# Performance work log

Measured on AMD Instinct MI355X. Metric: run time of the kernel, lower is better.

The kernel has to match this reference:

```python
import jax, jax.numpy as jnp
import numpy as np

H = 4    # heads
D = 64   # embed_dim


def setup_inputs() -> dict:
    key = jax.random.key(0)
    ks = jax.random.split(key, 10)
    N, L = 128, 1024
    f = jnp.float32
    return {
        "seq_items": jax.random.normal(ks[0], (N, L, D), f),
        "target_items": jax.random.normal(ks[1], (N, D), f),
        "memory": jax.random.normal(ks[2], (N, D), f),
        # nn.Linear weights stored torch-style [out_features, in_features]
        "Wk": jax.random.normal(ks[3], (H * D, D), f) * 0.1,
        "Wq": jax.random.normal(ks[4], (H * D, D), f) * 0.1,
        "Wv": jax.random.normal(ks[5], (H * D, D), f) * 0.1,
        "Wu": jax.random.normal(ks[6], (D, H * D), f) * 0.1,
        "bu": jnp.zeros((D,), f),
        "W1": jax.random.normal(ks[7], (8, 4 * D), f) * 0.1,
        "b1": jnp.zeros((8,), f),
        "W2": jax.random.normal(ks[8], (1, 8), f) * 0.1,
        "b2": jnp.zeros((1,), f),
    }


def reference(seq_items, target_items, memory, Wk, Wq, Wv, Wu, bu, W1, b1, W2, b2):
    N, L, d = seq_items.shape
    # projections, split into heads: [N, L, H, D]
    e = (seq_items @ Wk.T).reshape(N, L, H, D)
    V = (seq_items @ Wv.T).reshape(N, L, H, D)
    v = (target_items @ Wq.T).reshape(N, 1, H, D)   # broadcast over L
    m = memory.reshape(N, 1, 1, D)                   # broadcast over L and heads
    # np.where(e_, 1, 0): 1 where nonzero
    mask = (e != 0).astype(e.dtype)
    a1 = (v - e) * mask
    a2 = (v * e) * mask
    a3 = (m - e) * mask
    a4 = (m * e) * mask
    alpha = jnp.concatenate([a1, a2, a3, a4], axis=-1)  # [N, L, H, 4D]
    # tiny MLP attention scorer: 4D -> 8 -> 1, sigmoid each
    hmid = jax.nn.sigmoid(alpha @ W1.T + b1)
    att = jax.nn.sigmoid(hmid @ W2.T + b2)              # [N, L, H, 1]
    out = jnp.einsum('nlhq,nlhd->nqhd', att, V).reshape(N, H * D)
    output = out @ Wu.T + bu                            # [N, D]
    return output, att
```

## Files before the change

### kernel.cpp

```cpp
#include <hip/hip_runtime.h>
#include <math.h>

#define NN 128
#define LL 1024
#define HH 4
#define DD 64

typedef __attribute__((ext_vector_type(8))) short short8;
typedef __attribute__((ext_vector_type(4))) float f32x4;

__device__ __forceinline__ float sigm(float x) {
    return __builtin_amdgcn_rcpf(1.f + __expf(-x));
}

__device__ __forceinline__ unsigned short f2bf(float x) {
    union { float f; unsigned u; } v; v.f = x;
    unsigned r = v.u + 0x7FFFu + ((v.u >> 16) & 1u);
    return (unsigned short)(r >> 16);
}

__device__ __forceinline__ short8 pack_bf8(float4 a, float4 b) {
    short8 r;
    r[0] = (short)f2bf(a.x); r[1] = (short)f2bf(a.y);
    r[2] = (short)f2bf(a.z); r[3] = (short)f2bf(a.w);
    r[4] = (short)f2bf(b.x); r[5] = (short)f2bf(b.y);
    r[6] = (short)f2bf(b.z); r[7] = (short)f2bf(b.w);
    return r;
}

__global__ void __launch_bounds__(1024, 4) fused_kernel(
    const float* __restrict__ seq, const float* __restrict__ target,
    const float* __restrict__ memv, const float* __restrict__ Wk,
    const float* __restrict__ Wq, const float* __restrict__ Wv,
    const float* __restrict__ Wu, const float* __restrict__ bu,
    const float* __restrict__ W1, const float* __restrict__ b1,
    const float* __restrict__ W2, const float* __restrict__ b2,
    float* __restrict__ att_out, float* __restrict__ out)
{
    const int n = blockIdx.x;
    const int t = threadIdx.x;
    const int lane = t & 63;
    const int w = t >> 6;

    __shared__ __align__(16) float tl[64];
    __shared__ __align__(16) float ml[64];
    __shared__ float vh[4][64];
    __shared__ float wh[4][512];
    __shared__ float cp[4][64];
    __shared__ float cvl[32];
    __shared__ __align__(16) short wt_lds[32 * 72];
    __shared__ __align__(16) short seq_bf[256 * 72];
    __shared__ __align__(16) float att_l[1024];
    __shared__ __align__(16) float Tp_l[16][256];
    __shared__ float T_l[256];
    __shared__ __align__(16) float U_l[256];
    __shared__ float op[16 * 64];

    const int gg = t >> 8;
    const int tt = t & 255;
    const int h = gg;

    if (t < 64)       tl[t] = target[n * 64 + t];
    else if (t < 128) ml[t - 64] = memv[n * 64 + (t - 64)];
    __syncthreads();

    {
        const int d = tt >> 2, kq = tt & 3;
        const float4* wq4 = reinterpret_cast<const float4*>(Wq + (h * 64 + d) * 64 + kq * 16);
        const float4* tl4 = reinterpret_cast<const float4*>(tl + kq * 16);
        float s = 0.f;
        #pragma unroll
        for (int cc = 0; cc < 4; ++cc) {
            const float4 a = wq4[cc], bb = tl4[cc];
            s = fmaf(a.x, bb.x, s); s = fmaf(a.y, bb.y, s);
            s = fmaf(a.z, bb.z, s); s = fmaf(a.w, bb.w, s);
        }
        s += __shfl_xor(s, 1);
        s += __shfl_xor(s, 2);
        if (kq == 0) vh[h][d] = s;
    }
    __syncthreads();

    {
        const int d = tt & 63, jh = tt >> 6;
        const float vv = vh[h][d], mm = ml[d];
        #pragma unroll
        for (int r = 0; r < 2; ++r) {
            const int j = jh + r * 4;
            float wv = -W1[j * 256 + d] - W1[j * 256 + 128 + d];
            wv = fmaf(W1[j * 256 + 64 + d], vv, wv);
            wv = fmaf(W1[j * 256 + 192 + d], mm, wv);
            wh[h][d * 8 + j] = wv;
        }
    }
    if (tt < 64) {
        const int j = tt >> 3, sl = tt & 7;
        float s = 0.f;
        #pragma unroll
        for (int d8 = 0; d8 < 8; ++d8) {
            const int d = sl * 8 + d8;
            s = fmaf(W1[j * 256 + d], vh[h][d], s);
            s = fmaf(W1[j * 256 + 128 + d], ml[d], s);
        }
        cp[h][tt] = s;
    }
    __syncthreads();
    if (tt < 8) {
        float s = b1[tt];
        #pragma unroll
        for (int sl = 0; sl < 8; ++sl) s += cp[h][tt * 8 + sl];
        cvl[h * 8 + tt] = s;
    }

    {
        const int k = tt & 63, jp = tt >> 6;
        float s0 = 0.f, s1 = 0.f;
        #pragma unroll 8
        for (int d = 0; d < 64; ++d) {
            const float wk = Wk[(h * 64 + d) * 64 + k];
            s0 = fmaf(wk, wh[h][d * 8 + jp], s0);
            s1 = fmaf(wk, wh[h][d * 8 + jp + 4], s1);
        }
        wt_lds[(h * 8 + jp) * 72 + k]     = (short)f2bf(s0);
        wt_lds[(h * 8 + jp + 4) * 72 + k] = (short)f2bf(s1);
    }
    __syncthreads();

    const float* sbase = seq + (size_t)n * LL * 64;

    const int rt = w & 1;
    const int ctA = w >> 1;
    const int g = lane >> 4;
    const int cidx = lane & 15;

    short8 afrag[2];
    #pragma unroll
    for (int ks = 0; ks < 2; ++ks)
        afrag[ks] = *reinterpret_cast<const short8*>(
            wt_lds + (rt * 16 + cidx) * 72 + ks * 32 + g * 8);

    const float4 w2v = *reinterpret_cast<const float4*>(W2 + 4 * (g & 1));
    const float b2v = b2[0];
    const float cv0 = cvl[rt * 16 + g * 4 + 0];
    const float cv1 = cvl[rt * 16 + g * 4 + 1];
    const float cv2 = cvl[rt * 16 + g * 4 + 2];
    const float cv3 = cvl[rt * 16 + g * 4 + 3];

    float th0 = 0.f, th1 = 0.f, th2 = 0.f, th3 = 0.f;

    for (int sc = 0; sc < 4; ++sc) {
        const float* scb = sbase + sc * 256 * 64;

        #pragma unroll
        for (int gsg = 0; gsg < 2; ++gsg) {
            const int p8 = gsg * 1024 + t;
            const int l = p8 >> 3, seg = p8 & 7;
            const float* rp = scb + l * 64 + seg * 8;
            const float4 a = *reinterpret_cast<const float4*>(rp);
            const float4 bb = *reinterpret_cast<const float4*>(rp + 4);
            *reinterpret_cast<short8*>(seq_bf + l * 72 + seg * 8) = pack_bf8(a, bb);
        }
        __syncthreads();

        #pragma unroll
        for (int cc = 0; cc < 2; ++cc) {
            const int ct = ctA + cc * 8;
            const int l = ct * 16 + cidx;
            f32x4 acc;
            acc[0] = cv0; acc[1] = cv1; acc[2] = cv2; acc[3] = cv3;
            const short8 bf0 = *reinterpret_cast<const short8*>(seq_bf + l * 72 + g * 8);
            const short8 bf1 = *reinterpret_cast<const short8*>(seq_bf + l * 72 + 32 + g * 8);
            acc = __builtin_amdgcn_mfma_f32_16x16x32_bf16(afrag[0], bf0, acc, 0, 0, 0);
            acc = __builtin_amdgcn_mfma_f32_16x16x32_bf16(afrag[1], bf1, acc, 0, 0, 0);

            float local = w2v.x * sigm(acc[0]);
            local = fmaf(w2v.y, sigm(acc[1]), local);
            local = fmaf(w2v.z, sigm(acc[2]), local);
            local = fmaf(w2v.w, sigm(acc[3]), local);
            local += __shfl_xor(local, 16);
            const float attv = sigm(b2v + local);
            if ((lane & 16) == 0) {
                const int hh = 2 * rt + (g >> 1);
                att_l[l * 4 + hh] = attv;
            }
        }
        __syncthreads();

        att_out[((size_t)n * LL + sc * 256) * 4 + t] = att_l[t];

        {
            const float* sq = scb + (w * 16) * 64 + lane;
            #pragma unroll 4
            for (int li = 0; li < 16; ++li) {
                const float s = sq[li * 64];
                const float4 a = *reinterpret_cast<const float4*>(att_l + (w * 16 + li) * 4);
                th0 = fmaf(a.x, s, th0); th1 = fmaf(a.y, s, th1);
                th2 = fmaf(a.z, s, th2); th3 = fmaf(a.w, s, th3);
            }
        }
    }

    Tp_l[w][0 * 64 + lane] = th0;
    Tp_l[w][1 * 64 + lane] = th1;
    Tp_l[w][2 * 64 + lane] = th2;
    Tp_l[w][3 * 64 + lane] = th3;
    __syncthreads();

    if (t < 256) {
        float s = 0.f;
        #pragma unroll
        for (int i = 0; i < 16; ++i) s += Tp_l[i][t];
        T_l[t] = s;
    }
    __syncthreads();

    {
        const int hd = t >> 2, kq = t & 3;
        const int hq = hd >> 6;
        const float4* wv4 = reinterpret_cast<const float4*>(Wv + hd * 64 + kq * 16);
        const float4* t4  = reinterpret_cast<const float4*>(T_l + hq * 64 + kq * 16);
        float s = 0.f;
        #pragma unroll
        for (int i = 0; i < 4; ++i) {
            const float4 a = wv4[i], bb = t4[i];
            s = fmaf(a.x, bb.x, s); s = fmaf(a.y, bb.y, s);
            s = fmaf(a.z, bb.z, s); s = fmaf(a.w, bb.w, s);
        }
        s += __shfl_xor(s, 1);
        s += __shfl_xor(s, 2);
        if (kq == 0) U_l[hd] = s;
    }
    __syncthreads();

    {
        const int q = t & 63, qr = t >> 6;
        const float4* wu4 = reinterpret_cast<const float4*>(Wu + q * 256 + qr * 16);
        const float4* u4  = reinterpret_cast<const float4*>(U_l + qr * 16);
        float s = 0.f;
        #pragma unroll
        for (int i = 0; i < 4; ++i) {
            const float4 a = wu4[i], bb = u4[i];
            s = fmaf(a.x, bb.x, s); s = fmaf(a.y, bb.y, s);
            s = fmaf(a.z, bb.z, s); s = fmaf(a.w, bb.w, s);
        }
        op[qr * 64 + q] = s;
    }
    __syncthreads();
    if (t < 64) {
        float s = bu[t];
        #pragma unroll
        for (int qr = 0; qr < 16; ++qr) s += op[qr * 64 + t];
        out[n * 64 + t] = s;
    }
}

extern "C" void kernel_launch(void* const* d_in, const int* in_sizes, int n_in,
                              void* d_out, int out_size, void* d_ws, size_t ws_size,
                              hipStream_t stream) {
    const float* seq    = (const float*)d_in[0];
    const float* target = (const float*)d_in[1];
    const float* memv   = (const float*)d_in[2];
    const float* Wk     = (const float*)d_in[3];
    const float* Wq     = (const float*)d_in[4];
    const float* Wv     = (const float*)d_in[5];
    const float* Wu     = (const float*)d_in[6];
    const float* bu     = (const float*)d_in[7];
    const float* W1     = (const float*)d_in[8];
    const float* b1     = (const float*)d_in[9];
    const float* W2     = (const float*)d_in[10];
    const float* b2     = (const float*)d_in[11];

    float* out = (float*)d_out;
    float* att = out + NN * DD;

    fused_kernel<<<NN, 1024, 0, stream>>>(seq, target, memv, Wk, Wq, Wv, Wu,
                                          bu, W1, b1, W2, b2, att, out);
}
```

Baseline: 25.08 us.

## Split each sequence across four 256-thread blocks with a separate reduction kernel

Each batch row is now split into four blocks of 256 threads, each handling 256 sequence positions, instead of one 1024-thread block per row. The per-head weight preprocessing is recomputed in every block through a serial loop over heads. The second half-chunk of seq is prefetched into registers while the first half is processed. Partial outputs go to workspace and a second small kernel adds them together with the bias. The aim is better CU coverage with 512 smaller blocks, at the cost of redundant preprocessing work, an extra launch and a workspace round trip.

```diff
diff --git a/kernel.cpp b/kernel.cpp
--- a/kernel.cpp
+++ b/kernel.cpp
@@ -1,10 +1,9 @@
 #include <hip/hip_runtime.h>
+#include <hip/hip_bf16.h>
 #include <math.h>
 
 #define NN 128
 #define LL 1024
-#define HH 4
-#define DD 64
 
 typedef __attribute__((ext_vector_type(8))) short short8;
 typedef __attribute__((ext_vector_type(4))) float f32x4;
@@ -13,123 +12,121 @@
     return __builtin_amdgcn_rcpf(1.f + __expf(-x));
 }
 
-__device__ __forceinline__ unsigned short f2bf(float x) {
-    union { float f; unsigned u; } v; v.f = x;
-    unsigned r = v.u + 0x7FFFu + ((v.u >> 16) & 1u);
-    return (unsigned short)(r >> 16);
+__device__ __forceinline__ short bf16s(float x) {
+    __hip_bfloat16 h = __float2bfloat16(x);
+    union { __hip_bfloat16 hh; short s; } u; u.hh = h;
+    return u.s;
 }
 
 __device__ __forceinline__ short8 pack_bf8(float4 a, float4 b) {
     short8 r;
-    r[0] = (short)f2bf(a.x); r[1] = (short)f2bf(a.y);
-    r[2] = (short)f2bf(a.z); r[3] = (short)f2bf(a.w);
-    r[4] = (short)f2bf(b.x); r[5] = (short)f2bf(b.y);
-    r[6] = (short)f2bf(b.z); r[7] = (short)f2bf(b.w);
+    r[0] = bf16s(a.x); r[1] = bf16s(a.y); r[2] = bf16s(a.z); r[3] = bf16s(a.w);
+    r[4] = bf16s(b.x); r[5] = bf16s(b.y); r[6] = bf16s(b.z); r[7] = bf16s(b.w);
     return r;
 }
 
-__global__ void __launch_bounds__(1024, 4) fused_kernel(
+__global__ void __launch_bounds__(256, 2) fused_kernel(
     const float* __restrict__ seq, const float* __restrict__ target,
     const float* __restrict__ memv, const float* __restrict__ Wk,
     const float* __restrict__ Wq, const float* __restrict__ Wv,
-    const float* __restrict__ Wu, const float* __restrict__ bu,
-    const float* __restrict__ W1, const float* __restrict__ b1,
-    const float* __restrict__ W2, const float* __restrict__ b2,
-    float* __restrict__ att_out, float* __restrict__ out)
+    const float* __restrict__ Wu, const float* __restrict__ W1,
+    const float* __restrict__ b1, const float* __restrict__ W2,
+    const float* __restrict__ b2,
+    float* __restrict__ att_out, float* __restrict__ contrib)
 {
-    const int n = blockIdx.x;
+    const int b = blockIdx.x;
+    const int n = b >> 2;
+    const int c = b & 3;
     const int t = threadIdx.x;
     const int lane = t & 63;
     const int w = t >> 6;
 
     __shared__ __align__(16) float tl[64];
     __shared__ __align__(16) float ml[64];
-    __shared__ float vh[4][64];
-    __shared__ float wh[4][512];
-    __shared__ float cp[4][64];
+    __shared__ float vh[64];
+    __shared__ float wh[512];
+    __shared__ float cp[64];
     __shared__ float cvl[32];
     __shared__ __align__(16) short wt_lds[32 * 72];
-    __shared__ __align__(16) short seq_bf[256 * 72];
-    __shared__ __align__(16) float att_l[1024];
-    __shared__ __align__(16) float Tp_l[16][256];
+    __shared__ __align__(16) short seq_bf[128 * 72];
+    __shared__ __align__(16) float att_l[512];
+    __shared__ __align__(16) float Tp_l[4][256];
     __shared__ float T_l[256];
     __shared__ __align__(16) float U_l[256];
-    __shared__ float op[16 * 64];
-
-    const int gg = t >> 8;
-    const int tt = t & 255;
-    const int h = gg;
+    __shared__ float op[256];
 
     if (t < 64)       tl[t] = target[n * 64 + t];
     else if (t < 128) ml[t - 64] = memv[n * 64 + (t - 64)];
     __syncthreads();
 
-    {
-        const int d = tt >> 2, kq = tt & 3;
-        const float4* wq4 = reinterpret_cast<const float4*>(Wq + (h * 64 + d) * 64 + kq * 16);
-        const float4* tl4 = reinterpret_cast<const float4*>(tl + kq * 16);
-        float s = 0.f;
-        #pragma unroll
-        for (int cc = 0; cc < 4; ++cc) {
-            const float4 a = wq4[cc], bb = tl4[cc];
-            s = fmaf(a.x, bb.x, s); s = fmaf(a.y, bb.y, s);
-            s = fmaf(a.z, bb.z, s); s = fmaf(a.w, bb.w, s);
-        }
-        s += __shfl_xor(s, 1);
-        s += __shfl_xor(s, 2);
-        if (kq == 0) vh[h][d] = s;
-    }
-    __syncthreads();
-
-    {
-        const int d = tt & 63, jh = tt >> 6;
-        const float vv = vh[h][d], mm = ml[d];
-        #pragma unroll
-        for (int r = 0; r < 2; ++r) {
-            const int j = jh + r * 4;
-            float wv = -W1[j * 256 + d] - W1[j * 256 + 128 + d];
-            wv = fmaf(W1[j * 256 + 64 + d], vv, wv);
-            wv = fmaf(W1[j * 256 + 192 + d], mm, wv);
-            wh[h][d * 8 + j] = wv;
-        }
-    }
-    if (tt < 64) {
-        const int j = tt >> 3, sl = tt & 7;
-        float s = 0.f;
-        #pragma unroll
-        for (int d8 = 0; d8 < 8; ++d8) {
-            const int d = sl * 8 + d8;
-            s = fmaf(W1[j * 256 + d], vh[h][d], s);
-            s = fmaf(W1[j * 256 + 128 + d], ml[d], s);
-        }
-        cp[h][tt] = s;
-    }
-    __syncthreads();
-    if (tt < 8) {
-        float s = b1[tt];
-        #pragma unroll
-        for (int sl = 0; sl < 8; ++sl) s += cp[h][tt * 8 + sl];
-        cvl[h * 8 + tt] = s;
-    }
-
-    {
-        const int k = tt & 63, jp = tt >> 6;
-        float s0 = 0.f, s1 = 0.f;
-        #pragma unroll 8
-        for (int d = 0; d < 64; ++d) {
-            const float wk = Wk[(h * 64 + d) * 64 + k];
-            s0 = fmaf(wk, wh[h][d * 8 + jp], s0);
-            s1 = fmaf(wk, wh[h][d * 8 + jp + 4], s1);
-        }
-        wt_lds[(h * 8 + jp) * 72 + k]     = (short)f2bf(s0);
-        wt_lds[(h * 8 + jp + 4) * 72 + k] = (short)f2bf(s1);
-    }
-    __syncthreads();
-
-    const float* sbase = seq + (size_t)n * LL * 64;
+    for (int h = 0; h < 4; ++h) {
+        {
+            const int d = t >> 2, kq = t & 3;
+            const float4* wq4 = reinterpret_cast<const float4*>(Wq + (h * 64 + d) * 64 + kq * 16);
+            const float4* tl4 = reinterpret_cast<const float4*>(tl + kq * 16);
+            float s = 0.f;
+            #pragma unroll
+            for (int cc = 0; cc < 4; ++cc) {
+                const float4 a = wq4[cc], bb = tl4[cc];
+                s = fmaf(a.x, bb.x, s); s = fmaf(a.y, bb.y, s);
+                s = fmaf(a.z, bb.z, s); s = fmaf(a.w, bb.w, s);
+            }
+            s += __shfl_xor(s, 1);
+            s += __shfl_xor(s, 2);
+            if (kq == 0) vh[d] = s;
+        }
+        __syncthreads();
+
+        {
+            const int d = t & 63, jh = t >> 6;
+            const float vv = vh[d], mm = ml[d];
+            #pragma unroll
+            for (int r = 0; r < 2; ++r) {
+                const int j = jh + r * 4;
+                float wv = -W1[j * 256 + d] - W1[j * 256 + 128 + d];
+                wv = fmaf(W1[j * 256 + 64 + d], vv, wv);
+                wv = fmaf(W1[j * 256 + 192 + d], mm, wv);
+                wh[d * 8 + j] = wv;
+            }
+        }
+        if (t < 64) {
+            const int j = t >> 3, sl = t & 7;
+            float s = 0.f;
+            #pragma unroll
+            for (int d8 = 0; d8 < 8; ++d8) {
+                const int d = sl * 8 + d8;
+                s = fmaf(W1[j * 256 + d], vh[d], s);
+                s = fmaf(W1[j * 256 + 128 + d], ml[d], s);
+            }
+            cp[t] = s;
+        }
+        __syncthreads();
+
+        if (t < 8) {
+            float s = b1[t];
+            #pragma unroll
+            for (int sl = 0; sl < 8; ++sl) s += cp[t * 8 + sl];
+            cvl[h * 8 + t] = s;
+        }
+        {
+            const int k = t & 63, jp = t >> 6;
+            float s0 = 0.f, s1 = 0.f;
+            #pragma unroll 8
+            for (int d = 0; d < 64; ++d) {
+                const float wk = Wk[(h * 64 + d) * 64 + k];
+                s0 = fmaf(wk, wh[d * 8 + jp], s0);
+                s1 = fmaf(wk, wh[d * 8 + jp + 4], s1);
+            }
+            wt_lds[(h * 8 + jp) * 72 + k]     = bf16s(s0);
+            wt_lds[(h * 8 + jp + 4) * 72 + k] = bf16s(s1);
+        }
+        __syncthreads();
+    }
+
+    const float* sbase = seq + ((size_t)n * LL + c * 256) * 64;
 
     const int rt = w & 1;
-    const int ctA = w >> 1;
+    const int ctb = w >> 1;
     const int g = lane >> 4;
     const int cidx = lane & 15;
 
@@ -148,23 +145,38 @@
 
     float th0 = 0.f, th1 = 0.f, th2 = 0.f, th3 = 0.f;
 
-    for (int sc = 0; sc < 4; ++sc) {
-        const float* scb = sbase + sc * 256 * 64;
-
-        #pragma unroll
-        for (int gsg = 0; gsg < 2; ++gsg) {
-            const int p8 = gsg * 1024 + t;
+    {
+        #pragma unroll
+        for (int gg = 0; gg < 4; ++gg) {
+            const int p8 = gg * 256 + t;
             const int l = p8 >> 3, seg = p8 & 7;
-            const float* rp = scb + l * 64 + seg * 8;
+            const float* rp = sbase + l * 64 + seg * 8;
             const float4 a = *reinterpret_cast<const float4*>(rp);
             const float4 bb = *reinterpret_cast<const float4*>(rp + 4);
             *reinterpret_cast<short8*>(seq_bf + l * 72 + seg * 8) = pack_bf8(a, bb);
         }
-        __syncthreads();
-
-        #pragma unroll
-        for (int cc = 0; cc < 2; ++cc) {
-            const int ct = ctA + cc * 8;
+    }
+    float4 sw[8];
+    {
+        const float* scb1 = sbase + 128 * 64;
+        #pragma unroll
+        for (int gg = 0; gg < 4; ++gg) {
+            const int p8 = gg * 256 + t;
+            const int l = p8 >> 3, seg = p8 & 7;
+            const float* rp = scb1 + l * 64 + seg * 8;
+            sw[2 * gg]     = *reinterpret_cast<const float4*>(rp);
+            sw[2 * gg + 1] = *reinterpret_cast<const float4*>(rp + 4);
+        }
+    }
+    __syncthreads();
+
+    #pragma unroll
+    for (int sc = 0; sc < 2; ++sc) {
+        const float* scb = sbase + sc * 128 * 64;
+
+        #pragma unroll
+        for (int cc = 0; cc < 4; ++cc) {
+            const int ct = ctb + cc * 2;
             const int l = ct * 16 + cidx;
             f32x4 acc;
             acc[0] = cv0; acc[1] = cv1; acc[2] = cv2; acc[3] = cv3;
@@ -186,17 +198,32 @@
         }
         __syncthreads();
 
-        att_out[((size_t)n * LL + sc * 256) * 4 + t] = att_l[t];
-
-        {
-            const float* sq = scb + (w * 16) * 64 + lane;
+        {
+            float* dst = att_out + ((size_t)n * LL + c * 256 + sc * 128) * 4;
+            dst[t] = att_l[t];
+            dst[256 + t] = att_l[256 + t];
+        }
+
+        {
+            const float* sq = scb + (w * 32) * 64 + lane;
             #pragma unroll 4
-            for (int li = 0; li < 16; ++li) {
+            for (int li = 0; li < 32; ++li) {
                 const float s = sq[li * 64];
-                const float4 a = *reinterpret_cast<const float4*>(att_l + (w * 16 + li) * 4);
+                const float4 a = *reinterpret_cast<const float4*>(att_l + (w * 32 + li) * 4);
                 th0 = fmaf(a.x, s, th0); th1 = fmaf(a.y, s, th1);
                 th2 = fmaf(a.z, s, th2); th3 = fmaf(a.w, s, th3);
             }
+        }
+
+        if (sc == 0) {
+            #pragma unroll
+            for (int gg = 0; gg < 4; ++gg) {
+                const int p8 = gg * 256 + t;
+                const int l = p8 >> 3, seg = p8 & 7;
+                *reinterpret_cast<short8*>(seq_bf + l * 72 + seg * 8) =
+                    pack_bf8(sw[2 * gg], sw[2 * gg + 1]);
+            }
+            __syncthreads();
         }
     }
 
@@ -206,52 +233,56 @@
     Tp_l[w][3 * 64 + lane] = th3;
     __syncthreads();
 
-    if (t < 256) {
-        float s = 0.f;
-        #pragma unroll
-        for (int i = 0; i < 16; ++i) s += Tp_l[i][t];
-        T_l[t] = s;
-    }
+    T_l[t] = Tp_l[0][t] + Tp_l[1][t] + Tp_l[2][t] + Tp_l[3][t];
     __syncthreads();
 
     {
-        const int hd = t >> 2, kq = t & 3;
-        const int hq = hd >> 6;
-        const float4* wv4 = reinterpret_cast<const float4*>(Wv + hd * 64 + kq * 16);
-        const float4* t4  = reinterpret_cast<const float4*>(T_l + hq * 64 + kq * 16);
-        float s = 0.f;
-        #pragma unroll
-        for (int i = 0; i < 4; ++i) {
-            const float4 a = wv4[i], bb = t4[i];
-            s = fmaf(a.x, bb.x, s); s = fmaf(a.y, bb.y, s);
-            s = fmaf(a.z, bb.z, s); s = fmaf(a.w, bb.w, s);
-        }
-        s += __shfl_xor(s, 1);
-        s += __shfl_xor(s, 2);
-        if (kq == 0) U_l[hd] = s;
+        const int hd4 = t >> 2, kq = t & 3;
+        #pragma unroll
+        for (int r = 0; r < 4; ++r) {
+            const int hd = r * 64 + hd4;
+            const float4* wv4 = reinterpret_cast<const float4*>(Wv + hd * 64 + kq * 16);
+            const float4* t4  = reinterpret_cast<const float4*>(T_l + (hd >> 6) * 64 + kq * 16);
+            float s = 0.f;
+            #pragma unroll
+            for (int i = 0; i < 4; ++i) {
+                const float4 a = wv4[i], bb = t4[i];
+                s = fmaf(a.x, bb.x, s); s = fmaf(a.y, bb.y, s);
+                s = fmaf(a.z, bb.z, s); s = fmaf(a.w, bb.w, s);
+            }
+            s += __shfl_xor(s, 1);
+            s += __shfl_xor(s, 2);
+            if (kq == 0) U_l[hd] = s;
+        }
     }
     __syncthreads();
 
     {
         const int q = t & 63, qr = t >> 6;
-        const float4* wu4 = reinterpret_cast<const float4*>(Wu + q * 256 + qr * 16);
-        const float4* u4  = reinterpret_cast<const float4*>(U_l + qr * 16);
+        const float4* wu4 = reinterpret_cast<const float4*>(Wu + q * 256 + qr * 64);
+        const float4* u4  = reinterpret_cast<const float4*>(U_l + qr * 64);
         float s = 0.f;
         #pragma unroll
-        for (int i = 0; i < 4; ++i) {
+        for (int i = 0; i < 16; ++i) {
             const float4 a = wu4[i], bb = u4[i];
             s = fmaf(a.x, bb.x, s); s = fmaf(a.y, bb.y, s);
             s = fmaf(a.z, bb.z, s); s = fmaf(a.w, bb.w, s);
         }
-        op[qr * 64 + q] = s;
-    }
-    __syncthreads();
-    if (t < 64) {
-        float s = bu[t];
-        #pragma unroll
-        for (int qr = 0; qr < 16; ++qr) s += op[qr * 64 + t];
-        out[n * 64 + t] = s;
-    }
+        op[t] = s;
+    }
+    __syncthreads();
+    if (t < 64)
+        contrib[(n * 4 + c) * 64 + t] = op[t] + op[64 + t] + op[128 + t] + op[192 + t];
+}
+
+__global__ void __launch_bounds__(256) reduce_kernel(
+    const float* __restrict__ contrib, const float* __restrict__ bu,
+    float* __restrict__ out)
+{
+    const int idx = blockIdx.x * 256 + threadIdx.x;
+    const int n = idx >> 6, q = idx & 63;
+    out[idx] = bu[q] + contrib[(n * 4 + 0) * 64 + q] + contrib[(n * 4 + 1) * 64 + q]
+             + contrib[(n * 4 + 2) * 64 + q] + contrib[(n * 4 + 3) * 64 + q];
 }
 
 extern "C" void kernel_launch(void* const* d_in, const int* in_sizes, int n_in,
@@ -271,8 +302,11 @@
     const float* b2     = (const float*)d_in[11];
 
     float* out = (float*)d_out;
-    float* att = out + NN * DD;
-
-    fused_kernel<<<NN, 1024, 0, stream>>>(seq, target, memv, Wk, Wq, Wv, Wu,
-                                          bu, W1, b1, W2, b2, att, out);
-}
+    float* att = out + NN * 64;
+
+    float* contrib = (float*)d_ws;
+
+    fused_kernel<<<NN * 4, 256, 0, stream>>>(seq, target, memv, Wk, Wq, Wv, Wu,
+                                             W1, b1, W2, b2, att, contrib);
+    reduce_kernel<<<32, 256, 0, stream>>>(contrib, bu, out);
+}
```

Result: slower. 35.67 us (+42.2%).
